# Performance work log

Measured on AMD Instinct MI355X. Metric: run time of the kernel, lower is better.

The kernel has to match this reference:

```python
import jax, jax.numpy as jnp
import numpy as np
import math

D_MODEL = 1024
NUM_HEADS = 16
D_FF = 4096
EPS = 1e-5


def _linear_params(key, fan_in, fan_out):
    # torch nn.Linear default init: U(-1/sqrt(fan_in), 1/sqrt(fan_in))
    k1, k2 = jax.random.split(key)
    bound = 1.0 / math.sqrt(fan_in)
    W = jax.random.uniform(k1, (fan_in, fan_out), jnp.float32, -bound, bound)
    b = jax.random.uniform(k2, (fan_out,), jnp.float32, -bound, bound)
    return W, b


def setup_inputs() -> dict:
    key = jax.random.key(0)
    keys = jax.random.split(key, 16)
    src = jax.random.normal(keys[0], (4, 2048, D_MODEL), jnp.float32)
    tgt = jax.random.normal(keys[1], (4, 2048, D_MODEL), jnp.float32)
    sa_wq, sa_bq = _linear_params(keys[2], D_MODEL, D_MODEL)
    sa_wk, sa_bk = _linear_params(keys[3], D_MODEL, D_MODEL)
    sa_wv, sa_bv = _linear_params(keys[4], D_MODEL, D_MODEL)
    sa_wo, sa_bo = _linear_params(keys[5], D_MODEL, D_MODEL)
    ca_wq, ca_bq = _linear_params(keys[6], D_MODEL, D_MODEL)
    ca_wk, ca_bk = _linear_params(keys[7], D_MODEL, D_MODEL)
    ca_wv, ca_bv = _linear_params(keys[8], D_MODEL, D_MODEL)
    ca_wo, ca_bo = _linear_params(keys[9], D_MODEL, D_MODEL)
    ff_w1, ff_b1 = _linear_params(keys[10], D_MODEL, D_FF)
    ff_w2, ff_b2 = _linear_params(keys[11], D_FF, D_MODEL)
    ones = jnp.ones((D_MODEL,), jnp.float32)
    zeros = jnp.zeros((D_MODEL,), jnp.float32)
    return dict(
        src=src, tgt=tgt,
        sa_wq=sa_wq, sa_bq=sa_bq, sa_wk=sa_wk, sa_bk=sa_bk,
        sa_wv=sa_wv, sa_bv=sa_bv, sa_wo=sa_wo, sa_bo=sa_bo,
        ca_wq=ca_wq, ca_bq=ca_bq, ca_wk=ca_wk, ca_bk=ca_bk,
        ca_wv=ca_wv, ca_bv=ca_bv, ca_wo=ca_wo, ca_bo=ca_bo,
        ff_w1=ff_w1, ff_b1=ff_b1, ff_w2=ff_w2, ff_b2=ff_b2,
        ln1_g=ones, ln1_b=zeros, ln2_g=ones, ln2_b=zeros,
        ln3_g=ones, ln3_b=zeros,
    )


def _layernorm(x, g, b):
    mu = jnp.mean(x, axis=-1, keepdims=True)
    var = jnp.mean((x - mu) ** 2, axis=-1, keepdims=True)
    return (x - mu) * jax.lax.rsqrt(var + EPS) * g + b


def _mha(q_in, kv_in, wq, bq, wk, bk, wv, bv, wo, bo):
    B, Sq, D = q_in.shape
    Skv = kv_in.shape[1]
    H, dk = NUM_HEADS, D // NUM_HEADS
    Q = (q_in @ wq + bq).reshape(B, Sq, H, dk).transpose(0, 2, 1, 3)
    K = (kv_in @ wk + bk).reshape(B, Skv, H, dk).transpose(0, 2, 1, 3)
    V = (kv_in @ wv + bv).reshape(B, Skv, H, dk).transpose(0, 2, 1, 3)
    scores = jnp.einsum('bhqd,bhkd->bhqk', Q, K) / math.sqrt(dk)
    probs = jax.nn.softmax(scores, axis=-1)
    attn = jnp.einsum('bhqk,bhkd->bhqd', probs, V)
    attn = attn.transpose(0, 2, 1, 3).reshape(B, Sq, D)
    return attn @ wo + bo


def reference(src, tgt,
              sa_wq, sa_bq, sa_wk, sa_bk, sa_wv, sa_bv, sa_wo, sa_bo,
              ca_wq, ca_bq, ca_wk, ca_bk, ca_wv, ca_bv, ca_wo, ca_bo,
              ff_w1, ff_b1, ff_w2, ff_b2,
              ln1_g, ln1_b, ln2_g, ln2_b, ln3_g, ln3_b):
    # self-attention on tgt (dropout = identity in eval)
    sa = _mha(tgt, tgt, sa_wq, sa_bq, sa_wk, sa_bk, sa_wv, sa_bv, sa_wo, sa_bo)
    x = _layernorm(tgt + sa, ln1_g, ln1_b)
    # cross-attention: queries from decoder, keys/values from src
    ca = _mha(x, src, ca_wq, ca_bq, ca_wk, ca_bk, ca_wv, ca_bv, ca_wo, ca_bo)
    x = _layernorm(x + ca, ln2_g, ln2_b)
    # feed-forward
    ff = jax.nn.relu(x @ ff_w1 + ff_b1) @ ff_w2 + ff_b2
    x = _layernorm(x + ff, ln3_g, ln3_b)
    return x
```

## Files before the change

kernel.cpp:

```cpp
#include <hip/hip_runtime.h>
#include <hip/hip_bf16.h>
#include <stdint.h>


typedef __bf16 bf16_t;
typedef __bf16 bf16x8 __attribute__((ext_vector_type(8)));
typedef __bf16 bf16x4 __attribute__((ext_vector_type(4)));
typedef float  f32x4  __attribute__((ext_vector_type(4)));
typedef short  s16x4  __attribute__((ext_vector_type(4)));

#define SEQ_    2048
#define BATCH_  4
#define DM_     1024
#define NH_     16
#define DK_     64
#define DFF_    4096
#define TOK_    (BATCH_*SEQ_)
#define BH_     (BATCH_*NH_)
#define HEADEL_ ((size_t)BH_*SEQ_*DK_)

#define QSCALE_ 0.18033688011112042f

#define MFMA_BF16(a,b,c) __builtin_amdgcn_mfma_f32_16x16x32_bf16((a),(b),(c),0,0,0)
#define MFMA16(a,b,c) __builtin_amdgcn_mfma_f32_16x16x16bf16_1k((a),(b),(c),0,0,0)

static __device__ __forceinline__ void gl_lds16(const void* g, void* l) {
  __builtin_amdgcn_global_load_lds(
      (const __attribute__((address_space(1))) uint32_t*)g,
      (__attribute__((address_space(3))) uint32_t*)l, 16, 0, 0);
}

static __device__ __forceinline__ float fast_exp2(float x) {
#if __has_builtin(__builtin_amdgcn_exp2f)
  return __builtin_amdgcn_exp2f(x);
#else
  return exp2f(x);
#endif
}

__global__ __launch_bounds__(256) void cvt_bf16(const float* __restrict__ in,
                                                bf16_t* __restrict__ out, int n4) {
  int i = blockIdx.x * 256 + threadIdx.x;
  if (i < n4) {
    f32x4 v = *(const f32x4*)(in + (size_t)i * 4);
    bf16x4 o;
    o[0] = (bf16_t)v[0]; o[1] = (bf16_t)v[1]; o[2] = (bf16_t)v[2]; o[3] = (bf16_t)v[3];
    *(bf16x4*)(out + (size_t)i * 4) = o;
  }
}

__global__ __launch_bounds__(256) void transpose_w(const float* __restrict__ W,
                                                   bf16_t* __restrict__ Wt,
                                                   int K, int N) {
  __shared__ float t[32][33];
  int bx = blockIdx.x * 32;
  int by = blockIdx.y * 32;
  int tx = threadIdx.x;
  int ty = threadIdx.y;
  #pragma unroll
  for (int i = 0; i < 32; i += 8)
    t[ty + i][tx] = W[(size_t)(by + ty + i) * N + bx + tx];
  __syncthreads();
  #pragma unroll
  for (int i = 0; i < 32; i += 8)
    Wt[(size_t)(bx + ty + i) * K + by + tx] = (bf16_t)t[tx][ty + i];
}

__global__ __launch_bounds__(256) void gemm_bf16(
    const bf16_t* __restrict__ A, const bf16_t* __restrict__ Bt,
    const float* __restrict__ bias, const float* __restrict__ bias2,
    const float* __restrict__ bias3,
    float* outF, bf16_t* outB,
    int M, int N, int K, int mode, int relu, float scale)
{
  __shared__ __attribute__((aligned(16))) bf16_t lsA[128 * 32];
  __shared__ __attribute__((aligned(16))) bf16_t lsB[128 * 32];

  const int tid  = threadIdx.x;
  const int lane = tid & 63;
  const int w    = tid >> 6;
  const int q    = lane >> 4;
  const int r    = lane & 15;
  const int m0   = blockIdx.y * 128;
  const int n0   = blockIdx.x * 128;
  const int mb   = (w >> 1) * 64;
  const int nb   = (w & 1) * 64;

  f32x4 acc[4][4] = {};

  for (int k0 = 0; k0 < K; k0 += 32) {
    #pragma unroll
    for (int rr = 0; rr < 2; ++rr) {
      int flat = rr * 2048 + tid * 8;
      int row = flat >> 5, col = flat & 31;
      gl_lds16(A  + (size_t)(m0 + row) * K + k0 + col, &lsA[flat]);
      gl_lds16(Bt + (size_t)(n0 + row) * K + k0 + col, &lsB[flat]);
    }
    __syncthreads();
    bf16x8 af[4], bfr[4];
    #pragma unroll
    for (int mi = 0; mi < 4; ++mi)
      af[mi] = *(const bf16x8*)&lsA[(mb + mi * 16 + r) * 32 + q * 8];
    #pragma unroll
    for (int ni = 0; ni < 4; ++ni)
      bfr[ni] = *(const bf16x8*)&lsB[(nb + ni * 16 + r) * 32 + q * 8];
    #pragma unroll
    for (int mi = 0; mi < 4; ++mi)
      #pragma unroll
      for (int ni = 0; ni < 4; ++ni)
        acc[mi][ni] = MFMA_BF16(af[mi], bfr[ni], acc[mi][ni]);
    __syncthreads();
  }

  #pragma unroll
  for (int mi = 0; mi < 4; ++mi) {
    #pragma unroll
    for (int ni = 0; ni < 4; ++ni) {
      int col = n0 + nb + ni * 16 + r;
      float bv, sc = scale;
      int seg = 0, cw = col;
      if (mode == 3) {
        seg = col >> 10; cw = col & 1023;
        bv = (seg == 0) ? bias[cw] : ((seg == 1) ? bias2[cw] : bias3[cw]);
        if (seg != 0) sc = 1.f;
      } else if (mode == 4) {
        seg = col >> 10; cw = col & 1023;
        bv = (seg == 0) ? bias[cw] : bias2[cw];
      } else {
        bv = bias[col];
      }
      #pragma unroll
      for (int i = 0; i < 4; ++i) {
        int row = m0 + mb + mi * 16 + q * 4 + i;
        float v = (acc[mi][ni][i] + bv) * sc;
        if (relu) v = fmaxf(v, 0.f);
        if (outF) outF[(size_t)row * N + col] = v;
        if (outB) {
          size_t idx;
          if (mode == 0) {
            idx = (size_t)row * N + col;
          } else {
            int b = row >> 11, s = row & 2047, h = cw >> 6, d = cw & 63;
            bool vt;
            size_t base;
            if (mode == 1)      { vt = false; base = 0; }
            else if (mode == 2) { vt = true;  base = 0; }
            else if (mode == 3) { vt = (seg == 2); base = (size_t)seg * HEADEL_; }
            else                { vt = (seg == 1); base = (size_t)seg * HEADEL_; }
            if (!vt) idx = base + ((size_t)(b * NH_ + h) * SEQ_ + s) * DK_ + d;
            else     idx = base + ((size_t)(b * NH_ + h) * DK_ + d) * SEQ_ + s;
          }
          outB[idx] = (bf16_t)v;
        }
      }
    }
  }
}

__global__ __launch_bounds__(256) void flash_attn(
    const bf16_t* __restrict__ Q, const bf16_t* __restrict__ Kb,
    const bf16_t* __restrict__ Vt, bf16_t* __restrict__ O)
{
  __shared__ __attribute__((aligned(16))) bf16_t Kls[64 * 64];
  __shared__ __attribute__((aligned(16))) bf16_t Vls[64 * 64];

  const int tid  = threadIdx.x;
  const int w    = tid >> 6;
  const int lane = tid & 63;
  const int q    = lane >> 4;
  const int r    = lane & 15;
  const int bh   = blockIdx.y;
  const int q0   = blockIdx.x * 128 + w * 32;

  const bf16_t* Qp  = Q  + ((size_t)bh * SEQ_ + q0) * DK_;
  const bf16_t* Kp0 = Kb + (size_t)bh * SEQ_ * DK_;
  const bf16_t* Vp0 = Vt + (size_t)bh * DK_ * SEQ_;

  bf16x8 aq[2][2];
  #pragma unroll
  for (int rt = 0; rt < 2; ++rt)
    #pragma unroll
    for (int c = 0; c < 2; ++c)
      aq[rt][c] = *(const bf16x8*)(Qp + (rt * 16 + r) * DK_ + 32 * c + 8 * q);

  f32x4 o[2][4] = {};
  f32x4 l4[2] = {};

  const int srow0 = tid >> 3;
  const int scol0 = ((tid & 7) ^ (srow0 & 7)) * 8;
  const int srow1 = srow0 + 32;
  const int scol1 = ((tid & 7) ^ (srow1 & 7)) * 8;
  const int r7 = r & 7;

  for (int kv = 0; kv < SEQ_; kv += 64) {
    gl_lds16(Kp0 + (size_t)(kv + srow0) * DK_ + scol0, Kls + tid * 8);
    gl_lds16(Kp0 + (size_t)(kv + srow1) * DK_ + scol1, Kls + 2048 + tid * 8);
    gl_lds16(Vp0 + (size_t)srow0 * SEQ_ + kv + scol0, Vls + tid * 8);
    gl_lds16(Vp0 + (size_t)srow1 * SEQ_ + kv + scol1, Vls + 2048 + tid * 8);
    __syncthreads();

    bf16x8 kf[4][2];
    #pragma unroll
    for (int mt = 0; mt < 4; ++mt)
      #pragma unroll
      for (int c = 0; c < 2; ++c)
        kf[mt][c] = *(const bf16x8*)&Kls[(((16 * mt + r) * 8) + ((4 * c + q) ^ r7)) * 8];
    s16x4 vf[4][4];
    #pragma unroll
    for (int dt = 0; dt < 4; ++dt)
      #pragma unroll
      for (int mt = 0; mt < 4; ++mt)
        vf[dt][mt] = *(const s16x4*)&Vls[(((16 * dt + r) * 8) +
                        ((2 * mt + (q >> 1)) ^ r7)) * 8 + (q & 1) * 4];

    #pragma unroll
    for (int rt = 0; rt < 2; ++rt) {
      f32x4 st[4] = {};
      #pragma unroll
      for (int mt = 0; mt < 4; ++mt) {
        st[mt] = MFMA_BF16(kf[mt][0], aq[rt][0], st[mt]);
        st[mt] = MFMA_BF16(kf[mt][1], aq[rt][1], st[mt]);
      }
      s16x4 pf[4];
      f32x4 psum = {};
      #pragma unroll
      for (int mt = 0; mt < 4; ++mt) {
        f32x4 pe;
        #pragma unroll
        for (int i = 0; i < 4; ++i) pe[i] = fast_exp2(st[mt][i]);
        psum += pe;
        bf16x4 pb;
        #pragma unroll
        for (int i = 0; i < 4; ++i) pb[i] = (bf16_t)pe[i];
        pf[mt] = __builtin_bit_cast(s16x4, pb);
      }
      l4[rt] += psum;
      #pragma unroll
      for (int dt = 0; dt < 4; ++dt)
        #pragma unroll
        for (int mt = 0; mt < 4; ++mt)
          o[rt][dt] = MFMA16(vf[dt][mt], pf[mt], o[rt][dt]);
    }
    __syncthreads();
  }

  const int b = bh >> 4, h = bh & 15;
  #pragma unroll
  for (int rt = 0; rt < 2; ++rt) {
    float lr = (l4[rt][0] + l4[rt][1]) + (l4[rt][2] + l4[rt][3]);
    lr += __shfl_xor(lr, 16);
    lr += __shfl_xor(lr, 32);
    float linv = 1.f / lr;
    int token = b * SEQ_ + q0 + rt * 16 + r;
    #pragma unroll
    for (int dt = 0; dt < 4; ++dt) {
      bf16x4 ob;
      #pragma unroll
      for (int i = 0; i < 4; ++i) ob[i] = (bf16_t)(o[rt][dt][i] * linv);
      *(bf16x4*)(O + (size_t)token * DM_ + h * DK_ + 16 * dt + 4 * q) = ob;
    }
  }
}

__global__ __launch_bounds__(256) void resid_ln(
    const float* A, const float* Bv,
    const float* g, const float* be,
    float* outF, bf16_t* outB)
{
  const int w = threadIdx.x >> 6, lane = threadIdx.x & 63;
  const int row = blockIdx.x * 4 + w;
  const float* a = A  + (size_t)row * DM_;
  const float* b = Bv + (size_t)row * DM_;
  float v[16];
  float s = 0.f;
  #pragma unroll
  for (int c = 0; c < 4; ++c) {
    f32x4 x = *(const f32x4*)(a + c * 256 + lane * 4);
    f32x4 y = *(const f32x4*)(b + c * 256 + lane * 4);
    #pragma unroll
    for (int k = 0; k < 4; ++k) { v[c * 4 + k] = x[k] + y[k]; s += v[c * 4 + k]; }
  }
  s += __shfl_xor(s, 1);  s += __shfl_xor(s, 2);  s += __shfl_xor(s, 4);
  s += __shfl_xor(s, 8);  s += __shfl_xor(s, 16); s += __shfl_xor(s, 32);
  float mu = s * (1.f / DM_);
  float ss = 0.f;
  #pragma unroll
  for (int k = 0; k < 16; ++k) { float d = v[k] - mu; ss += d * d; }
  ss += __shfl_xor(ss, 1);  ss += __shfl_xor(ss, 2);  ss += __shfl_xor(ss, 4);
  ss += __shfl_xor(ss, 8);  ss += __shfl_xor(ss, 16); ss += __shfl_xor(ss, 32);
  float rstd = rsqrtf(ss * (1.f / DM_) + 1e-5f);
  #pragma unroll
  for (int c = 0; c < 4; ++c) {
    int idx = c * 256 + lane * 4;
    f32x4 gg = *(const f32x4*)(g + idx);
    f32x4 bb = *(const f32x4*)(be + idx);
    f32x4 ov; bf16x4 ob;
    #pragma unroll
    for (int k = 0; k < 4; ++k) {
      float val = (v[c * 4 + k] - mu) * rstd * gg[k] + bb[k];
      ov[k] = val; ob[k] = (bf16_t)val;
    }
    *(f32x4*)(outF + (size_t)row * DM_ + idx) = ov;
    if (outB) *(bf16x4*)(outB + (size_t)row * DM_ + idx) = ob;
  }
}

extern "C" void kernel_launch(void* const* d_in, const int* in_sizes, int n_in,
                              void* d_out, int out_size, void* d_ws, size_t ws_size,
                              hipStream_t stream)
{
  (void)in_sizes; (void)n_in; (void)out_size; (void)ws_size;
  const float* src   = (const float*)d_in[0];
  const float* tgt   = (const float*)d_in[1];
  const float* sa_wq = (const float*)d_in[2];  const float* sa_bq = (const float*)d_in[3];
  const float* sa_wk = (const float*)d_in[4];  const float* sa_bk = (const float*)d_in[5];
  const float* sa_wv = (const float*)d_in[6];  const float* sa_bv = (const float*)d_in[7];
  const float* sa_wo = (const float*)d_in[8];  const float* sa_bo = (const float*)d_in[9];
  const float* ca_wq = (const float*)d_in[10]; const float* ca_bq = (const float*)d_in[11];
  const float* ca_wk = (const float*)d_in[12]; const float* ca_bk = (const float*)d_in[13];
  const float* ca_wv = (const float*)d_in[14]; const float* ca_bv = (const float*)d_in[15];
  const float* ca_wo = (const float*)d_in[16]; const float* ca_bo = (const float*)d_in[17];
  const float* ff_w1 = (const float*)d_in[18]; const float* ff_b1 = (const float*)d_in[19];
  const float* ff_w2 = (const float*)d_in[20]; const float* ff_b2 = (const float*)d_in[21];
  const float* ln1g  = (const float*)d_in[22]; const float* ln1b  = (const float*)d_in[23];
  const float* ln2g  = (const float*)d_in[24]; const float* ln2b  = (const float*)d_in[25];
  const float* ln3g  = (const float*)d_in[26]; const float* ln3b  = (const float*)d_in[27];

  char* p = (char*)d_ws;
  auto alloc = [&](size_t bytes) -> char* {
    char* r = p; p += (bytes + 255) & ~(size_t)255; return r;
  };

  const size_t ACT_B  = (size_t)TOK_ * DM_ * 2;
  const size_t W_B    = (size_t)DM_ * DM_ * 2;
  const size_t HEAD_B = HEADEL_ * 2;

  bf16_t* tgt_bf = (bf16_t*)alloc(ACT_B);
  bf16_t* src_bf = (bf16_t*)alloc(ACT_B);
  bf16_t* wt_saq = (bf16_t*)alloc(W_B);
  bf16_t* wt_sak = (bf16_t*)alloc(W_B);
  bf16_t* wt_sav = (bf16_t*)alloc(W_B);
  bf16_t* wt_sao = (bf16_t*)alloc(W_B);
  bf16_t* wt_caq = (bf16_t*)alloc(W_B);
  bf16_t* wt_cak = (bf16_t*)alloc(W_B);
  bf16_t* wt_cav = (bf16_t*)alloc(W_B);
  bf16_t* wt_cao = (bf16_t*)alloc(W_B);
  bf16_t* w1t    = (bf16_t*)alloc((size_t)DFF_ * DM_ * 2);
  bf16_t* w2t    = (bf16_t*)alloc((size_t)DM_ * DFF_ * 2);
  char*   Rg     = alloc((size_t)TOK_ * DFF_ * 2);
  bf16_t* Qb     = (bf16_t*)Rg;
  bf16_t* Kbuf   = (bf16_t*)(Rg + HEAD_B);
  bf16_t* Vtb    = (bf16_t*)(Rg + 2 * HEAD_B);
  bf16_t* attnO  = (bf16_t*)(Rg + 3 * HEAD_B);
  bf16_t* hbuf   = (bf16_t*)Rg;
  float*  x1F    = (float*)alloc((size_t)TOK_ * DM_ * 4);
  bf16_t* x1B    = (bf16_t*)alloc(ACT_B);
  float*  x2F    = (float*)alloc((size_t)TOK_ * DM_ * 4);
  bf16_t* x2B    = (bf16_t*)alloc(ACT_B);
  float*  yF     = (float*)d_out;

  const int n4 = TOK_ * DM_ / 4;
  cvt_bf16<<<n4 / 256, 256, 0, stream>>>(tgt, tgt_bf, n4);
  cvt_bf16<<<n4 / 256, 256, 0, stream>>>(src, src_bf, n4);

  dim3 tb(32, 8);
  transpose_w<<<dim3(32, 32), tb, 0, stream>>>(sa_wq, wt_saq, DM_, DM_);
  transpose_w<<<dim3(32, 32), tb, 0, stream>>>(sa_wk, wt_sak, DM_, DM_);
  transpose_w<<<dim3(32, 32), tb, 0, stream>>>(sa_wv, wt_sav, DM_, DM_);
  transpose_w<<<dim3(32, 32), tb, 0, stream>>>(sa_wo, wt_sao, DM_, DM_);
  transpose_w<<<dim3(32, 32), tb, 0, stream>>>(ca_wq, wt_caq, DM_, DM_);
  transpose_w<<<dim3(32, 32), tb, 0, stream>>>(ca_wk, wt_cak, DM_, DM_);
  transpose_w<<<dim3(32, 32), tb, 0, stream>>>(ca_wv, wt_cav, DM_, DM_);
  transpose_w<<<dim3(32, 32), tb, 0, stream>>>(ca_wo, wt_cao, DM_, DM_);
  transpose_w<<<dim3(128, 32), tb, 0, stream>>>(ff_w1, w1t, DM_, DFF_);
  transpose_w<<<dim3(32, 128), tb, 0, stream>>>(ff_w2, w2t, DFF_, DM_);

  dim3 g1(DM_ / 128, TOK_ / 128);
  dim3 g3(3 * DM_ / 128, TOK_ / 128);
  dim3 g2(2 * DM_ / 128, TOK_ / 128);
  dim3 gf(DFF_ / 128, TOK_ / 128);
  dim3 ga(SEQ_ / 128, BH_);

  gemm_bf16<<<g3, 256, 0, stream>>>(tgt_bf, wt_saq, sa_bq, sa_bk, sa_bv,
                                    nullptr, Qb, TOK_, 3 * DM_, DM_, 3, 0, QSCALE_);
  flash_attn<<<ga, 256, 0, stream>>>(Qb, Kbuf, Vtb, attnO);
  gemm_bf16<<<g1, 256, 0, stream>>>(attnO, wt_sao, sa_bo, nullptr, nullptr,
                                    yF, nullptr, TOK_, DM_, DM_, 0, 0, 1.f);
  resid_ln<<<TOK_ / 4, 256, 0, stream>>>(tgt, yF, ln1g, ln1b, x1F, x1B);

  gemm_bf16<<<g1, 256, 0, stream>>>(x1B, wt_caq, ca_bq, nullptr, nullptr,
                                    nullptr, Qb, TOK_, DM_, DM_, 1, 0, QSCALE_);
  gemm_bf16<<<g2, 256, 0, stream>>>(src_bf, wt_cak, ca_bk, ca_bv, nullptr,
                                    nullptr, Kbuf, TOK_, 2 * DM_, DM_, 4, 0, 1.f);
  flash_attn<<<ga, 256, 0, stream>>>(Qb, Kbuf, Vtb, attnO);
  gemm_bf16<<<g1, 256, 0, stream>>>(attnO, wt_cao, ca_bo, nullptr, nullptr,
                                    yF, nullptr, TOK_, DM_, DM_, 0, 0, 1.f);
  resid_ln<<<TOK_ / 4, 256, 0, stream>>>(x1F, yF, ln2g, ln2b, x2F, x2B);

  gemm_bf16<<<gf, 256, 0, stream>>>(x2B, w1t, ff_b1, nullptr, nullptr,
                                    nullptr, hbuf, TOK_, DFF_, DM_, 0, 1, 1.f);
  gemm_bf16<<<g1, 256, 0, stream>>>(hbuf, w2t, ff_b2, nullptr, nullptr,
                                    yF, nullptr, TOK_, DM_, DFF_, 0, 0, 1.f);
  resid_ln<<<TOK_ / 4, 256, 0, stream>>>(x2F, yF, ln3g, ln3b, (float*)d_out, nullptr);
}
```

Baseline: 1.007 ms.

## Swizzle GEMM and attention block order and double the GEMM K-step

The GEMM now remaps its linear block index so that groups of 8 row-tiles run next to each other, which should raise L2 reuse of the shared B/A tiles. Each loop iteration also stages two 32-wide K slices into separate LDS buffers before one barrier pair, so the number of __syncthreads per K is halved. The flash-attention kernel remaps blocks so that consecutive block IDs spread across heads, placing the 8 heads that share a group on the same XCD via the low bits. This relies on grid dimensions being multiples of 8 and on K being divisible by 64. The GEMM also uses twice the LDS, which may reduce occupancy.

```diff
diff --git a/kernel.cpp b/kernel.cpp
--- a/kernel.cpp
+++ b/kernel.cpp
@@ -73,42 +73,58 @@
     float* outF, bf16_t* outB,
     int M, int N, int K, int mode, int relu, float scale)
 {
-  __shared__ __attribute__((aligned(16))) bf16_t lsA[128 * 32];
-  __shared__ __attribute__((aligned(16))) bf16_t lsB[128 * 32];
+  __shared__ __attribute__((aligned(16))) bf16_t lsA[2][128 * 32];
+  __shared__ __attribute__((aligned(16))) bf16_t lsB[2][128 * 32];
 
   const int tid  = threadIdx.x;
   const int lane = tid & 63;
   const int w    = tid >> 6;
   const int q    = lane >> 4;
   const int r    = lane & 15;
-  const int m0   = blockIdx.y * 128;
-  const int n0   = blockIdx.x * 128;
+
+  const int gx = gridDim.x;
+  const int b  = blockIdx.y * gx + blockIdx.x;
+  const int t_ = b >> 3;
+  const int bm = (t_ / gx) * 8 + (b & 7);
+  const int bn = t_ % gx;
+  const int m0 = bm * 128;
+  const int n0 = bn * 128;
+
   const int mb   = (w >> 1) * 64;
   const int nb   = (w & 1) * 64;
 
   f32x4 acc[4][4] = {};
 
-  for (int k0 = 0; k0 < K; k0 += 32) {
-    #pragma unroll
-    for (int rr = 0; rr < 2; ++rr) {
-      int flat = rr * 2048 + tid * 8;
-      int row = flat >> 5, col = flat & 31;
-      gl_lds16(A  + (size_t)(m0 + row) * K + k0 + col, &lsA[flat]);
-      gl_lds16(Bt + (size_t)(n0 + row) * K + k0 + col, &lsB[flat]);
+  const int srow = tid >> 3;
+  const int scol = (tid & 7) * 8 + 0;
+
+  for (int k0 = 0; k0 < K; k0 += 64) {
+    #pragma unroll
+    for (int h = 0; h < 2; ++h) {
+      #pragma unroll
+      for (int rr = 0; rr < 2; ++rr) {
+        int flat = rr * 2048 + tid * 8;
+        int row = flat >> 5, col = flat & 31;
+        gl_lds16(A  + (size_t)(m0 + row) * K + k0 + 32 * h + col, &lsA[h][flat]);
+        gl_lds16(Bt + (size_t)(n0 + row) * K + k0 + 32 * h + col, &lsB[h][flat]);
+      }
     }
     __syncthreads();
-    bf16x8 af[4], bfr[4];
-    #pragma unroll
-    for (int mi = 0; mi < 4; ++mi)
-      af[mi] = *(const bf16x8*)&lsA[(mb + mi * 16 + r) * 32 + q * 8];
-    #pragma unroll
-    for (int ni = 0; ni < 4; ++ni)
-      bfr[ni] = *(const bf16x8*)&lsB[(nb + ni * 16 + r) * 32 + q * 8];
-    #pragma unroll
-    for (int mi = 0; mi < 4; ++mi)
+    #pragma unroll
+    for (int h = 0; h < 2; ++h) {
+      bf16x8 af[4], bfr[4];
+      #pragma unroll
+      for (int mi = 0; mi < 4; ++mi)
+        af[mi] = *(const bf16x8*)&lsA[h][(mb + mi * 16 + r) * 32 + q * 8];
       #pragma unroll
       for (int ni = 0; ni < 4; ++ni)
-        acc[mi][ni] = MFMA_BF16(af[mi], bfr[ni], acc[mi][ni]);
+        bfr[ni] = *(const bf16x8*)&lsB[h][(nb + ni * 16 + r) * 32 + q * 8];
+      #pragma unroll
+      for (int mi = 0; mi < 4; ++mi)
+        #pragma unroll
+        for (int ni = 0; ni < 4; ++ni)
+          acc[mi][ni] = MFMA_BF16(af[mi], bfr[ni], acc[mi][ni]);
+    }
     __syncthreads();
   }
 
@@ -140,15 +156,15 @@
           if (mode == 0) {
             idx = (size_t)row * N + col;
           } else {
-            int b = row >> 11, s = row & 2047, h = cw >> 6, d = cw & 63;
+            int bb = row >> 11, s = row & 2047, h = cw >> 6, d = cw & 63;
             bool vt;
             size_t base;
             if (mode == 1)      { vt = false; base = 0; }
             else if (mode == 2) { vt = true;  base = 0; }
             else if (mode == 3) { vt = (seg == 2); base = (size_t)seg * HEADEL_; }
             else                { vt = (seg == 1); base = (size_t)seg * HEADEL_; }
-            if (!vt) idx = base + ((size_t)(b * NH_ + h) * SEQ_ + s) * DK_ + d;
-            else     idx = base + ((size_t)(b * NH_ + h) * DK_ + d) * SEQ_ + s;
+            if (!vt) idx = base + ((size_t)(bb * NH_ + h) * SEQ_ + s) * DK_ + d;
+            else     idx = base + ((size_t)(bb * NH_ + h) * DK_ + d) * SEQ_ + s;
           }
           outB[idx] = (bf16_t)v;
         }
@@ -169,8 +185,10 @@
   const int lane = tid & 63;
   const int q    = lane >> 4;
   const int r    = lane & 15;
-  const int bh   = blockIdx.y;
-  const int q0   = blockIdx.x * 128 + w * 32;
+
+  const int bl   = blockIdx.y * gridDim.x + blockIdx.x;
+  const int bh   = (bl & 7) * 8 + ((bl >> 3) & 7);
+  const int q0   = (bl >> 6) * 128 + w * 32;
 
   const bf16_t* Qp  = Q  + ((size_t)bh * SEQ_ + q0) * DK_;
   const bf16_t* Kp0 = Kb + (size_t)bh * SEQ_ * DK_;
```

Result: faster. 981.8 us (-2.5%).
